# Kernel optimization log

Hardware: AMD Instinct MI355X
Metric: run time of the kernel (lower is better)

Reference implementation:

```python
import jax, jax.numpy as jnp
import numpy as np

B, H, W, C = 8, 64, 64, 512
DQK = C // 8  # query/key channel dim from Conv2D(filters//8, 1)


def setup_inputs() -> dict:
    key = jax.random.key(0)
    ks = jax.random.split(key, 8)
    s_in = 1.0 / np.sqrt(C)
    x = jax.random.normal(ks[0], (B, H, W, C), dtype=jnp.float32)
    Wq = jax.random.normal(ks[1], (C, DQK), dtype=jnp.float32) * s_in
    bq = jnp.zeros((DQK,), dtype=jnp.float32)
    Wk = jax.random.normal(ks[2], (C, DQK), dtype=jnp.float32) * s_in
    bk = jnp.zeros((DQK,), dtype=jnp.float32)
    Wv = jax.random.normal(ks[3], (C, C), dtype=jnp.float32) * s_in
    bv = jnp.zeros((C,), dtype=jnp.float32)
    # gamma initialized to zeros in the original, but use a nonzero value so
    # the attention branch actually contributes to the output/gradients.
    gamma = jnp.ones((1,), dtype=jnp.float32) * 0.5
    return {"x": x, "Wq": Wq, "bq": bq, "Wk": Wk, "bk": bk,
            "Wv": Wv, "bv": bv, "gamma": gamma}


def reference(x, Wq, bq, Wk, bk, Wv, bv, gamma):
    b, h, w, c = x.shape
    n = h * w  # spatial_size
    xf = x.reshape(b, n, c)
    # 1x1 convs == per-pixel channel matmuls
    q = xf @ Wq + bq            # [B, N, C//8]
    k = xf @ Wk + bk            # [B, N, C//8]
    v = xf @ Wv + bv            # [B, N, C]
    # Dot(axes=-1): attn[b,i,j] = sum_d q[b,i,d] * k[b,j,d]
    attn = jnp.einsum('bid,bjd->bij', q, k)
    attn = jax.nn.softmax(attn, axis=-1)
    # Dot(axes=-2): out[b,j,c] = sum_i attn[b,i,j] * v[b,i,c]  (note transpose)
    out = jnp.einsum('bij,bic->bjc', attn, v)
    out = out.reshape(b, h, w, c)
    return gamma * out + x
```

## Files before the change

kernel.cpp:

```cpp
#include <hip/hip_runtime.h>
#include <hip/hip_bf16.h>
#include <cstdio>

typedef unsigned short u16;
typedef __attribute__((ext_vector_type(4))) float f32x4;
typedef __attribute__((ext_vector_type(8))) short s16x8;

#define LOG2E 1.4426950408889634f

__device__ __forceinline__ u16 bf16b(float f) {
  union { float f; unsigned u; } c; c.f = f;
  unsigned u = c.u;
  return (u16)((u + 0x7FFFu + ((u >> 16) & 1u)) >> 16);
}

__device__ __forceinline__ void load16(const void* g, void* l) {
  __builtin_amdgcn_global_load_lds(
      (const __attribute__((address_space(1))) void*)g,
      (__attribute__((address_space(3))) void*)l, 16, 0, 0);
}


__global__ __launch_bounds__(256) void cvt_all_k(const float* __restrict__ x,
                                                 const float* __restrict__ Wq,
                                                 const float* __restrict__ Wk,
                                                 const float* __restrict__ Wv,
                                                 u16* __restrict__ xb,
                                                 u16* __restrict__ Wcat) {
  int bid = blockIdx.x;
  if (bid < 16384) {
    long i = ((long)bid * 256 + threadIdx.x) * 4;
    float4 f = *(const float4*)&x[i];
    unsigned lo = (unsigned)bf16b(f.x) | ((unsigned)bf16b(f.y) << 16);
    unsigned hi = (unsigned)bf16b(f.z) | ((unsigned)bf16b(f.w) << 16);
    uint2 v; v.x = lo; v.y = hi;
    *(uint2*)&xb[i] = v;
  } else {
    int idx = (bid - 16384) * 256 + threadIdx.x;
    int nn = idx >> 9, k = idx & 511;
    float v;
    if (nn < 64)       v = Wq[k * 64 + nn];
    else if (nn < 128) v = Wk[k * 64 + (nn - 64)];
    else               v = Wv[k * 512 + (nn - 128)];
    Wcat[idx] = bf16b(v);
  }
}

__global__ __launch_bounds__(256, 2) void projGemm(
    const u16* __restrict__ A, const u16* __restrict__ B,
    u16* __restrict__ Qb, u16* __restrict__ Kb, u16* __restrict__ Vt,
    const float* __restrict__ bq, const float* __restrict__ bk,
    const float* __restrict__ bv) {
  constexpr int BM = 128, BN = 128, FM = 4, FN = 4;
  __shared__ __align__(16) u16 At[BM * 64];
  __shared__ __align__(16) u16 Bt[BN * 64];
  const int tid = threadIdx.x;
  const int lane = tid & 63, w = tid >> 6;
  const int wr = w >> 1, wc = w & 1;
  const int l15 = lane & 15, lhi = lane >> 4;
  const long m0 = (long)blockIdx.x * BM;
  const long n0 = (long)blockIdx.y * BN;

  f32x4 acc[FM][FN] = {};

  for (int k0 = 0; k0 < 512; k0 += 64) {
#pragma unroll
    for (int it = 0; it < 8; ++it) {
      int q = it * 256 + tid;
      if (q < BM * 8) {
        int row = q >> 3, c8 = q & 7;
        load16(A + (m0 + row) * 512 + k0 + c8 * 8, &At[q * 8]);
      } else {
        int q2 = q - BM * 8;
        int row = q2 >> 3, c8 = q2 & 7;
        load16(B + (n0 + row) * 512 + k0 + c8 * 8, &Bt[q2 * 8]);
      }
    }
    __syncthreads();
#pragma unroll
    for (int kk = 0; kk < 64; kk += 32) {
      s16x8 af[FM], bf[FN];
#pragma unroll
      for (int i = 0; i < FM; ++i)
        af[i] = *(const s16x8*)&At[(wr * 64 + i * 16 + l15) * 64 + kk + lhi * 8];
#pragma unroll
      for (int j = 0; j < FN; ++j)
        bf[j] = *(const s16x8*)&Bt[(wc * 64 + j * 16 + l15) * 64 + kk + lhi * 8];
#pragma unroll
      for (int i = 0; i < FM; ++i)
#pragma unroll
        for (int j = 0; j < FN; ++j)
          acc[i][j] = __builtin_amdgcn_mfma_f32_16x16x32_bf16(af[i], bf[j],
                                                              acc[i][j], 0, 0, 0);
    }
    __syncthreads();
  }

#pragma unroll
  for (int i = 0; i < FM; ++i) {
#pragma unroll
    for (int j = 0; j < FN; ++j) {
      long mm = m0 + wr * 64 + i * 16 + lhi * 4;
      long nn = n0 + wc * 64 + j * 16 + l15;
      if (nn < 64) {
        float bb = bq[nn];
#pragma unroll
        for (int r = 0; r < 4; ++r)
          Qb[(mm + r) * 64 + nn] = bf16b(acc[i][j][r] + bb);
      } else if (nn < 128) {
        float bb = bk[nn - 64];
#pragma unroll
        for (int r = 0; r < 4; ++r)
          Kb[(mm + r) * 64 + nn - 64] = bf16b(acc[i][j][r] + bb);
      } else {
        long c = nn - 128;
        float bb = bv[c];
        unsigned u01 = (unsigned)bf16b(acc[i][j][0] + bb) |
                       ((unsigned)bf16b(acc[i][j][1] + bb) << 16);
        unsigned u23 = (unsigned)bf16b(acc[i][j][2] + bb) |
                       ((unsigned)bf16b(acc[i][j][3] + bb) << 16);
        uint2 u; u.x = u01; u.y = u23;
        *(uint2*)&Vt[(mm >> 12) * 512 * 4096 + c * 4096 + (mm & 4095)] = u;
      }
    }
  }
}

__global__ __launch_bounds__(256, 2) void stats_k(const u16* __restrict__ Qb,
                                                  const u16* __restrict__ Kb,
                                                  float* __restrict__ m_part,
                                                  float* __restrict__ l_part) {
  const int s = blockIdx.x + 32 * (blockIdx.y + 4 * blockIdx.z);
  const int b = s & 7;
  const int rest = s >> 3;
  const int jc = rest >> 5;
  const long i0 = (long)(rest & 31) * 128;
  const u16* Q = Qb + (long)b * 4096 * 64;
  const u16* Kp = Kb + (long)b * 4096 * 64;
  __shared__ __align__(16) u16 Qt[128 * 64];
  __shared__ __align__(16) u16 Kt[128 * 64];
  const int tid = threadIdx.x, lane = tid & 63, w = tid >> 6;
  const int l15 = lane & 15, lhi = lane >> 4;

#pragma unroll
  for (int it = 0; it < 4; ++it) {
    int q = it * 256 + tid;
    int row = q >> 3, c8 = q & 7;
    load16(Q + (i0 + row) * 64 + c8 * 8, &Qt[q * 8]);
  }

  float mrun[2][4], lrun[2][4];
#pragma unroll
  for (int i = 0; i < 2; ++i)
#pragma unroll
    for (int r = 0; r < 4; ++r) { mrun[i][r] = -1e30f; lrun[i][r] = 0.f; }

  for (int jt = 0; jt < 8; ++jt) {
    long j0 = (long)jc * 1024 + jt * 128;
#pragma unroll
    for (int it = 0; it < 4; ++it) {
      int q = it * 256 + tid;
      int row = q >> 3, c8 = q & 7;
      load16(Kp + (j0 + row) * 64 + c8 * 8, &Kt[q * 8]);
    }
    __syncthreads();
    f32x4 acc[2][8] = {};
#pragma unroll
    for (int kk = 0; kk < 64; kk += 32) {
      s16x8 af[2], bf[8];
#pragma unroll
      for (int i = 0; i < 2; ++i)
        af[i] = *(const s16x8*)&Qt[(w * 32 + i * 16 + l15) * 64 + kk + lhi * 8];
#pragma unroll
      for (int j = 0; j < 8; ++j)
        bf[j] = *(const s16x8*)&Kt[(j * 16 + l15) * 64 + kk + lhi * 8];
#pragma unroll
      for (int i = 0; i < 2; ++i)
#pragma unroll
        for (int j = 0; j < 8; ++j)
          acc[i][j] = __builtin_amdgcn_mfma_f32_16x16x32_bf16(af[i], bf[j],
                                                              acc[i][j], 0, 0, 0);
    }
#pragma unroll
    for (int i = 0; i < 2; ++i)
#pragma unroll
      for (int r = 0; r < 4; ++r) {
        float tm = acc[i][0][r];
#pragma unroll
        for (int j = 1; j < 8; ++j) tm = fmaxf(tm, acc[i][j][r]);
        float mo = mrun[i][r];
        float mn = fmaxf(mo, tm);
        float s2 = 0.f;
#pragma unroll
        for (int j = 0; j < 8; ++j) s2 += __expf(acc[i][j][r] - mn);
        lrun[i][r] = lrun[i][r] * __expf(mo - mn) + s2;
        mrun[i][r] = mn;
      }
    __syncthreads();
  }

#pragma unroll
  for (int i = 0; i < 2; ++i)
#pragma unroll
    for (int r = 0; r < 4; ++r) {
      float m = mrun[i][r], l = lrun[i][r];
#pragma unroll
      for (int d = 1; d < 16; d <<= 1) {
        float mo = __shfl_xor(m, d);
        float lo = __shfl_xor(l, d);
        float mn = fmaxf(m, mo);
        l = l * __expf(m - mn) + lo * __expf(mo - mn);
        m = mn;
      }
      if (l15 == 0) {
        long ig = i0 + w * 32 + i * 16 + lhi * 4 + r;
        long idx = ((long)(b * 4 + jc)) * 4096 + ig;
        m_part[idx] = m;
        l_part[idx] = l;
      }
    }
}

__global__ __launch_bounds__(256) void merge_k(const float* __restrict__ m_part,
                                               const float* __restrict__ l_part,
                                               float* __restrict__ mfin) {
  int idx = blockIdx.x * 256 + threadIdx.x;
  int b = idx >> 12, i = idx & 4095;
  float m = -1e30f, l = 0.f;
#pragma unroll
  for (int jc = 0; jc < 4; ++jc) {
    long o = ((long)(b * 4 + jc)) * 4096 + i;
    float mp = m_part[o], lp = l_part[o];
    float mn = fmaxf(m, mp);
    l = l * __expf(m - mn) + lp * __expf(mp - mn);
    m = mn;
  }
  mfin[idx] = fmaf(m, LOG2E, __log2f(l));
}

__global__ __launch_bounds__(512, 2) void fusedPV(
    const u16* __restrict__ Qb, const u16* __restrict__ Kb,
    const u16* __restrict__ Vt, const float* __restrict__ mfin,
    const float* __restrict__ x, const float* __restrict__ gamma,
    float* __restrict__ out) {
  __shared__ __align__(16) u16 Vc[2][512 * 64];
  __shared__ __align__(16) u16 Pl[2][128 * 64];
  const int tid = threadIdx.x, lane = tid & 63, w = tid >> 6;
  const int l15 = lane & 15, lhi = lane >> 4;
  const int wi = w & 1, wj = w >> 1;
  const int wjj = w & 1, wcc = w >> 1;
  const int s = blockIdx.x + 32 * blockIdx.z;
  const int pi = (s & 7) * 32 + (s >> 3);
  const int b = pi >> 5;
  const long j0 = (long)(pi & 31) * 128;
  const u16* Qg = Qb + (long)b * 4096 * 64;
  const u16* Kg = Kb + (long)b * 4096 * 64;
  const u16* Vg = Vt + (long)b * 512 * 4096;
  const float* mg = mfin + (long)b * 4096;
  const float gma = gamma[0];

#pragma unroll
  for (int p = 0; p < 2; ++p) {
    int q = p * 512 + tid;
    int r = q >> 3, col = q & 7, cg = col ^ (r & 7);
    load16(Kg + (j0 + r) * 64 + cg * 8,
           (char*)&Pl[0][0] + r * 128 + col * 16);
  }
  asm volatile("s_waitcnt vmcnt(0) lgkmcnt(0)\n\ts_barrier" ::: "memory");
  s16x8 kf[2][2];
#pragma unroll
  for (int fj = 0; fj < 2; ++fj)
#pragma unroll
    for (int kx = 0; kx < 2; ++kx) {
      int r = wj * 32 + fj * 16 + l15;
      kf[fj][kx] = *(const s16x8*)((const char*)&Pl[0][0] + r * 128 +
                                   (((kx * 32 + lhi * 8) * 2) ^ ((r & 7) << 4)));
    }
  __syncthreads();

  f32x4 acc2[4][8] = {};
  s16x8 qf[2][2];
  f32x4 mv[2];

#pragma unroll
  for (int fi = 0; fi < 2; ++fi) {
#pragma unroll
    for (int kx = 0; kx < 2; ++kx)
      qf[fi][kx] = *(const s16x8*)&Qg[(long)(wi * 32 + fi * 16 + l15) * 64 +
                                      kx * 32 + lhi * 8];
    mv[fi] = *(const f32x4*)&mg[wi * 32 + fi * 16 + lhi * 4];
  }
#pragma unroll
  for (int p = 0; p < 8; ++p) {
    int q = p * 512 + tid;
    int r = q >> 3, col = q & 7, cg = col ^ (r & 7);
    load16(Vg + (long)r * 4096 + cg * 8,
           (char*)&Vc[0][0] + r * 128 + col * 16);
  }
#pragma unroll
  for (int fi = 0; fi < 2; ++fi) {
    f32x4 a1[2] = {};
#pragma unroll
    for (int kx = 0; kx < 2; ++kx)
#pragma unroll
      for (int fj = 0; fj < 2; ++fj)
        a1[fj] = __builtin_amdgcn_mfma_f32_16x16x32_bf16(qf[fi][kx],
                                                         kf[fj][kx], a1[fj],
                                                         0, 0, 0);
    const int i0l = wi * 32 + fi * 16 + lhi * 4;
#pragma unroll
    for (int fj = 0; fj < 2; ++fj) {
      int j = wj * 32 + fj * 16 + l15;
      float p0 = __builtin_amdgcn_exp2f(fmaf(a1[fj][0], LOG2E, -mv[fi][0]));
      float p1 = __builtin_amdgcn_exp2f(fmaf(a1[fj][1], LOG2E, -mv[fi][1]));
      float p2 = __builtin_amdgcn_exp2f(fmaf(a1[fj][2], LOG2E, -mv[fi][2]));
      float p3 = __builtin_amdgcn_exp2f(fmaf(a1[fj][3], LOG2E, -mv[fi][3]));
      uint2 u;
      u.x = (unsigned)bf16b(p0) | ((unsigned)bf16b(p1) << 16);
      u.y = (unsigned)bf16b(p2) | ((unsigned)bf16b(p3) << 16);
      *(uint2*)((char*)&Pl[0][0] + j * 128 + ((i0l * 2) ^ ((j & 7) << 4))) = u;
    }
  }

  for (int t = 0; t < 64; ++t) {
    const char* plc = (const char*)&Pl[t & 1][0];
    char* pln = (char*)&Pl[(t + 1) & 1][0];
    const char* vcc = (const char*)&Vc[t & 1][0];
    asm volatile("s_waitcnt vmcnt(0) lgkmcnt(0)\n\ts_barrier" ::: "memory");
    if (t < 63) {
      const long i2 = (long)(t + 1) * 64;
#pragma unroll
      for (int fi = 0; fi < 2; ++fi) {
#pragma unroll
        for (int kx = 0; kx < 2; ++kx)
          qf[fi][kx] = *(const s16x8*)&Qg[(i2 + wi * 32 + fi * 16 + l15) * 64 +
                                          kx * 32 + lhi * 8];
        mv[fi] = *(const f32x4*)&mg[i2 + wi * 32 + fi * 16 + lhi * 4];
      }
#pragma unroll
      for (int p = 0; p < 8; ++p) {
        int q = p * 512 + tid;
        int r = q >> 3, col = q & 7, cg = col ^ (r & 7);
        load16(Vg + (long)r * 4096 + i2 + cg * 8,
               (char*)&Vc[(t + 1) & 1][0] + r * 128 + col * 16);
      }
    }
    __builtin_amdgcn_sched_barrier(0);
    __builtin_amdgcn_s_setprio(1);
#pragma unroll
    for (int kx = 0; kx < 2; ++kx) {
      s16x8 pa[4];
#pragma unroll
      for (int fm = 0; fm < 4; ++fm) {
        int r = wjj * 64 + fm * 16 + l15;
        pa[fm] = *(const s16x8*)(plc + r * 128 +
                                 (((kx * 32 + lhi * 8) * 2) ^ ((r & 7) << 4)));
      }
#pragma unroll
      for (int fn = 0; fn < 8; ++fn) {
        int r = wcc * 128 + fn * 16 + l15;
        s16x8 vb = *(const s16x8*)(vcc + r * 128 +
                                   (((kx * 32 + lhi * 8) * 2) ^ ((r & 7) << 4)));
#pragma unroll
        for (int fm = 0; fm < 4; ++fm)
          acc2[fm][fn] = __builtin_amdgcn_mfma_f32_16x16x32_bf16(
              pa[fm], vb, acc2[fm][fn], 0, 0, 0);
      }
    }
    __builtin_amdgcn_s_setprio(0);
    if (t < 63) {
#pragma unroll
      for (int fi = 0; fi < 2; ++fi) {
        f32x4 a1[2] = {};
#pragma unroll
        for (int kx = 0; kx < 2; ++kx)
#pragma unroll
          for (int fj = 0; fj < 2; ++fj)
            a1[fj] = __builtin_amdgcn_mfma_f32_16x16x32_bf16(qf[fi][kx],
                                                             kf[fj][kx],
                                                             a1[fj], 0, 0, 0);
        const int i0l = wi * 32 + fi * 16 + lhi * 4;
#pragma unroll
        for (int fj = 0; fj < 2; ++fj) {
          int j = wj * 32 + fj * 16 + l15;
          float p0 = __builtin_amdgcn_exp2f(fmaf(a1[fj][0], LOG2E, -mv[fi][0]));
          float p1 = __builtin_amdgcn_exp2f(fmaf(a1[fj][1], LOG2E, -mv[fi][1]));
          float p2 = __builtin_amdgcn_exp2f(fmaf(a1[fj][2], LOG2E, -mv[fi][2]));
          float p3 = __builtin_amdgcn_exp2f(fmaf(a1[fj][3], LOG2E, -mv[fi][3]));
          uint2 u;
          u.x = (unsigned)bf16b(p0) | ((unsigned)bf16b(p1) << 16);
          u.y = (unsigned)bf16b(p2) | ((unsigned)bf16b(p3) << 16);
          *(uint2*)(pln + j * 128 + ((i0l * 2) ^ ((j & 7) << 4))) = u;
        }
      }
    }
  }

#pragma unroll
  for (int fm = 0; fm < 4; ++fm) {
#pragma unroll
    for (int fn = 0; fn < 8; ++fn) {
      long j = j0 + wjj * 64 + fm * 16 + lhi * 4;
      long c = wcc * 128 + fn * 16 + l15;
#pragma unroll
      for (int r = 0; r < 4; ++r) {
        long o = ((long)b * 4096 + j + r) * 512 + c;
        out[o] = gma * acc2[fm][fn][r] + x[o];
      }
    }
  }
}


extern "C" void kernel_launch(void* const* d_in, const int* in_sizes, int n_in,
                              void* d_out, int out_size, void* d_ws,
                              size_t ws_size, hipStream_t stream) {
  const float* x = (const float*)d_in[0];
  const float* Wq = (const float*)d_in[1];
  const float* bq = (const float*)d_in[2];
  const float* Wk = (const float*)d_in[3];
  const float* bk = (const float*)d_in[4];
  const float* Wv = (const float*)d_in[5];
  const float* bv = (const float*)d_in[6];
  const float* gamma = (const float*)d_in[7];
  float* out = (float*)d_out;

  char* ws = (char*)d_ws;
  size_t off = 0;
  auto alloc = [&](size_t bytes) {
    char* p = ws + off;
    off += (bytes + 255) & ~(size_t)255;
    return p;
  };
  u16* xb = (u16*)alloc((size_t)32768 * 512 * 2);
  u16* Wcat = (u16*)alloc((size_t)640 * 512 * 2);
  u16* Qb = (u16*)alloc((size_t)8 * 4096 * 64 * 2);
  u16* Kb = (u16*)alloc((size_t)8 * 4096 * 64 * 2);
  u16* Vt = (u16*)alloc((size_t)8 * 512 * 4096 * 2);
  float* m_part = (float*)alloc((size_t)8 * 4 * 4096 * 4);
  float* l_part = (float*)alloc((size_t)8 * 4 * 4096 * 4);
  float* mfin = (float*)alloc((size_t)8 * 4096 * 4);
  if (off > ws_size) {
    fprintf(stderr, "kernel_launch: ws too small: need %zu have %zu\n", off,
            ws_size);
    return;
  }

  cvt_all_k<<<16384 + 1280, 256, 0, stream>>>(x, Wq, Wk, Wv, xb, Wcat);
  projGemm<<<dim3(256, 5, 1), 256, 0, stream>>>(xb, Wcat, Qb, Kb, Vt, bq, bk,
                                                bv);
  stats_k<<<dim3(32, 4, 8), 256, 0, stream>>>(Qb, Kb, m_part, l_part);
  merge_k<<<128, 256, 0, stream>>>(m_part, l_part, mfin);
  fusedPV<<<dim3(32, 1, 8), 512, 0, stream>>>(Qb, Kb, Vt, mfin, x, gamma,
                                              out);
}
```

Baseline: 285.0 us.

## Double-buffer LDS tiles in projection GEMM to overlap loads with MFMA

Makes the A/B shared-memory tiles in the QKV projection GEMM double-buffered. The next k-slice is prefetched with global_load_lds while MFMAs run on the current slice, and the two syncthreads are replaced with one explicit waitcnt+barrier. This aims to hide global-memory latency behind compute, at the cost of doubling LDS usage per block, which could reduce occupancy.

```diff
diff --git a/kernel.cpp b/kernel.cpp
--- a/kernel.cpp
+++ b/kernel.cpp
@@ -52,8 +52,8 @@
     const float* __restrict__ bq, const float* __restrict__ bk,
     const float* __restrict__ bv) {
   constexpr int BM = 128, BN = 128, FM = 4, FN = 4;
-  __shared__ __align__(16) u16 At[BM * 64];
-  __shared__ __align__(16) u16 Bt[BN * 64];
+  __shared__ __align__(16) u16 At[2][BM * 64];
+  __shared__ __align__(16) u16 Bt[2][BN * 64];
   const int tid = threadIdx.x;
   const int lane = tid & 63, w = tid >> 6;
   const int wr = w >> 1, wc = w & 1;
@@ -63,29 +63,48 @@
 
   f32x4 acc[FM][FN] = {};
 
-  for (int k0 = 0; k0 < 512; k0 += 64) {
-#pragma unroll
-    for (int it = 0; it < 8; ++it) {
-      int q = it * 256 + tid;
-      if (q < BM * 8) {
-        int row = q >> 3, c8 = q & 7;
-        load16(A + (m0 + row) * 512 + k0 + c8 * 8, &At[q * 8]);
-      } else {
-        int q2 = q - BM * 8;
-        int row = q2 >> 3, c8 = q2 & 7;
-        load16(B + (n0 + row) * 512 + k0 + c8 * 8, &Bt[q2 * 8]);
-      }
-    }
-    __syncthreads();
+#pragma unroll
+  for (int it = 0; it < 8; ++it) {
+    int q = it * 256 + tid;
+    if (q < BM * 8) {
+      int row = q >> 3, c8 = q & 7;
+      load16(A + (m0 + row) * 512 + c8 * 8, &At[0][q * 8]);
+    } else {
+      int q2 = q - BM * 8;
+      int row = q2 >> 3, c8 = q2 & 7;
+      load16(B + (n0 + row) * 512 + c8 * 8, &Bt[0][q2 * 8]);
+    }
+  }
+
+  for (int ks = 0; ks < 8; ++ks) {
+    const int cur = ks & 1;
+    asm volatile("s_waitcnt vmcnt(0) lgkmcnt(0)\n\ts_barrier" ::: "memory");
+    if (ks < 7) {
+      const int k1 = (ks + 1) * 64;
+#pragma unroll
+      for (int it = 0; it < 8; ++it) {
+        int q = it * 256 + tid;
+        if (q < BM * 8) {
+          int row = q >> 3, c8 = q & 7;
+          load16(A + (m0 + row) * 512 + k1 + c8 * 8, &At[cur ^ 1][q * 8]);
+        } else {
+          int q2 = q - BM * 8;
+          int row = q2 >> 3, c8 = q2 & 7;
+          load16(B + (n0 + row) * 512 + k1 + c8 * 8, &Bt[cur ^ 1][q2 * 8]);
+        }
+      }
+    }
 #pragma unroll
     for (int kk = 0; kk < 64; kk += 32) {
       s16x8 af[FM], bf[FN];
 #pragma unroll
       for (int i = 0; i < FM; ++i)
-        af[i] = *(const s16x8*)&At[(wr * 64 + i * 16 + l15) * 64 + kk + lhi * 8];
+        af[i] = *(const s16x8*)&At[cur][(wr * 64 + i * 16 + l15) * 64 + kk +
+                                       lhi * 8];
 #pragma unroll
       for (int j = 0; j < FN; ++j)
-        bf[j] = *(const s16x8*)&Bt[(wc * 64 + j * 16 + l15) * 64 + kk + lhi * 8];
+        bf[j] = *(const s16x8*)&Bt[cur][(wc * 64 + j * 16 + l15) * 64 + kk +
+                                        lhi * 8];
 #pragma unroll
       for (int i = 0; i < FM; ++i)
 #pragma unroll
@@ -93,7 +112,6 @@
           acc[i][j] = __builtin_amdgcn_mfma_f32_16x16x32_bf16(af[i], bf[j],
                                                               acc[i][j], 0, 0, 0);
     }
-    __syncthreads();
   }
 
 #pragma unroll
```

Measured after the change: 291.2 us. 2.2% more time.
